# Performance work log

Measured on AMD Instinct MI355X. Metric: run time of the kernel, lower is better.

The kernel has to match this reference:

```python
import jax, jax.numpy as jnp
import numpy as np

N_PATCH, N_Z, K, BS = 16, 128, 10, 1024
D = N_PATCH * N_Z


def setup_inputs() -> dict:
    key = jax.random.key(0)
    k1, k2, k3, k4 = jax.random.split(key, 4)
    z = jax.random.normal(k1, (BS, D), dtype=jnp.float32)
    m = jax.random.normal(k2, (K, D), dtype=jnp.float32)
    L = jax.random.normal(k3, (K, D, D), dtype=jnp.float32)
    components = jax.random.randint(k4, (BS,), 0, K, dtype=jnp.int64)
    return {"z": z, "m": m, "L": L, "components": components}


def reference(z, m, L, components):
    # samps[k] = m[k] + z @ L[k].T   -> (K, BS, D)
    samps = jnp.einsum('bd,ked->kbe', z, L) + m[:, None, :]
    # one-hot mask-and-sum over components == gather selected expert per sample
    x = samps[components, jnp.arange(z.shape[0])]  # (BS, D)
    return x.reshape(-1, N_PATCH, N_Z)
```

## Files before the change

### kernel.cpp

```cpp
#include <hip/hip_runtime.h>
#include <hip/hip_bf16.h>


#define DDIM  2048
#define BSAMP 1024
#define KCOMP 10
#define MPAD  160
#define NT    32
#define BK    32
#define NITER (DDIM / BK)
#define TILEP 12288
#define ABYTES 12288
#define BBYTES 4096
#define STAGE_BYTES (ABYTES + BBYTES)
#define NBUF  3

typedef __attribute__((ext_vector_type(8))) short bf16x8;
typedef __attribute__((ext_vector_type(4))) float f32x4;

__device__ __forceinline__ void async16(void* lds, const void* g) {
    __builtin_amdgcn_global_load_lds(
        (const __attribute__((address_space(1))) void*)g,
        (__attribute__((address_space(3))) void*)lds, 16, 0, 0);
}

__device__ __forceinline__ short bfs(float x) {
    __hip_bfloat16 h = __float2bfloat16(x);
    return *reinterpret_cast<short*>(&h);
}

__global__ void build_map(const int* __restrict__ comp,
                          int* __restrict__ rowmap,
                          int* __restrict__ counts) {
    __shared__ int sc[KCOMP];
    const int t = threadIdx.x;
    if (t < KCOMP) sc[t] = 0;
    __syncthreads();
    const int c = comp[t];
    const int r = atomicAdd(&sc[c], 1);
    if (r < MPAD) rowmap[c * MPAD + r] = t;
    __syncthreads();
    if (t < KCOMP) counts[t] = sc[t];
}

__global__ void zgather(const float* __restrict__ z,
                        const int* __restrict__ rowmap,
                        short* __restrict__ zb) {
    const int k  = blockIdx.x;
    const int sp = blockIdx.y;
    const int t  = threadIdx.x;
    const int c  = t & 7;
    const int g  = c & 3;
    const int s0 = rowmap[k * MPAD + 2 * sp]     & (BSAMP - 1);
    const int s1 = rowmap[k * MPAD + 2 * sp + 1] & (BSAMP - 1);
    const int src = (c >> 2) ? s1 : s0;
    const int swz = (c ^ (sp & 7)) * 16;
    char* kbase = (char*)zb + (size_t)k * NITER * TILEP + sp * 128 + swz;
#pragma unroll
    for (int p = 0; p < 2; ++p) {
        const int it = p * 32 + (t >> 3);
        const float* zr = z + (size_t)src * DDIM + it * BK + g * 8;
        f32x4 x = *(const f32x4*)zr;
        f32x4 y = *(const f32x4*)(zr + 4);
        bf16x8 r;
#pragma unroll
        for (int i = 0; i < 4; ++i) { r[i] = bfs(x[i]); r[4 + i] = bfs(y[i]); }
        *(bf16x8*)(kbase + (size_t)it * TILEP) = r;
    }
}

__global__ __launch_bounds__(256, 3)
void gmm_gemm(const short* __restrict__ zb,
              const float* __restrict__ mvec,
              const float* __restrict__ Lmat,
              const int* __restrict__ rowmap,
              const int* __restrict__ counts,
              float* __restrict__ out) {
    __shared__ __attribute__((aligned(16))) char smem[NBUF * STAGE_BYTES];
    const int t    = threadIdx.x;
    const int lane = t & 63;
    const int w    = t >> 6;
    const int mh   = w >> 1;
    const int nh   = w & 1;
    const int k    = blockIdx.y;
    const int n0   = blockIdx.x * NT;
    const float* Lk = Lmat + (size_t)k * DDIM * DDIM;
    const char* zt  = (const char*)zb + (size_t)k * NITER * TILEP;
    const int cnt  = counts[k];

    int mtmax = (cnt - mh * 80 + 15) >> 4;
    mtmax = mtmax < 0 ? 0 : (mtmax > 5 ? 5 : mtmax);

    const int br = t >> 3,          bc = ((t & 7) ^ (br & 7)) * 4;
    const unsigned ub = (unsigned)(t & ~63) * 16;

    auto stage = [&](int bi, int it) {
        char* lb = smem + bi * STAGE_BYTES;
        const char* at = zt + (size_t)it * TILEP;
        async16(lb + ub,          at + t * 16);
        async16(lb + 4096 + ub,   at + 4096 + t * 16);
        async16(lb + 8192 + ub,   at + 8192 + t * 16);
        async16(lb + ABYTES + ub, Lk + (size_t)(n0 + br) * DDIM + it * BK + bc);
    };

    f32x4 acc[5];
#pragma unroll
    for (int mt = 0; mt < 5; ++mt) acc[mt] = (f32x4){0.f, 0.f, 0.f, 0.f};

    const int fr = lane & 15;
    const int g  = lane >> 4;
    const int rb = nh * 16 + fr;
    const int h0 = ((2 * g)     ^ (rb & 7)) * 4;
    const int h1 = ((2 * g + 1) ^ (rb & 7)) * 4;
    const int frh = fr >> 1;
    const int fra = (fr & 1) * 4 + g;
    const int abase = (mh * 40 + frh) * 128 + ((fra ^ frh) * 16);

    auto compute = [&](int bi) {
        const char* lb = smem + bi * STAGE_BYTES;
        const float* B = (const float*)(lb + ABYTES);
        f32x4 x = *(const f32x4*)(B + rb * 32 + h0);
        f32x4 y = *(const f32x4*)(B + rb * 32 + h1);
        bf16x8 bb;
#pragma unroll
        for (int i = 0; i < 4; ++i) { bb[i] = bfs(x[i]); bb[4 + i] = bfs(y[i]); }
#pragma unroll
        for (int mt = 0; mt < 5; ++mt) {
            if (mt < mtmax) {
                bf16x8 a = *(const bf16x8*)(lb + abase + mt * 1024);
                acc[mt] = __builtin_amdgcn_mfma_f32_16x16x32_bf16(a, bb, acc[mt], 0, 0, 0);
            }
        }
    };

    stage(0, 0); stage(1, 1); stage(2, 2);
    int bi = 0;
    for (int it = 0; it < NITER - 2; ++it) {
        asm volatile("s_waitcnt vmcnt(8)" ::: "memory");
        __builtin_amdgcn_s_barrier();
        compute(bi);
        __builtin_amdgcn_s_barrier();
        if (it + 3 < NITER) stage(bi, it + 3);
        bi = (bi == NBUF - 1) ? 0 : bi + 1;
    }
    asm volatile("s_waitcnt vmcnt(4)" ::: "memory");
    __builtin_amdgcn_s_barrier();
    compute(bi);
    __builtin_amdgcn_s_barrier();
    bi = (bi == NBUF - 1) ? 0 : bi + 1;
    asm volatile("s_waitcnt vmcnt(0)" ::: "memory");
    __builtin_amdgcn_s_barrier();
    compute(bi);

    const int rquad = g * 4;
    const int e  = n0 + nh * 16 + fr;
    const float mu = mvec[k * DDIM + e];
#pragma unroll
    for (int mt = 0; mt < 5; ++mt) {
        if (mt < mtmax) {
            const int sb = mh * 80 + mt * 16 + rquad;
#pragma unroll
            for (int r = 0; r < 4; ++r) {
                const int slot = sb + r;
                if (slot < cnt) {
                    const int b = rowmap[k * MPAD + slot];
                    out[(size_t)b * DDIM + e] = acc[mt][r] + mu;
                }
            }
        }
    }
}

extern "C" void kernel_launch(void* const* d_in, const int* in_sizes, int n_in,
                              void* d_out, int out_size, void* d_ws, size_t ws_size,
                              hipStream_t stream) {
    const float* z    = (const float*)d_in[0];
    const float* mvec = (const float*)d_in[1];
    const float* Lmat = (const float*)d_in[2];
    const int* comp   = (const int*)d_in[3];
    float* out        = (float*)d_out;

    int* rowmap = (int*)d_ws;
    int* counts = rowmap + KCOMP * MPAD;
    short* zb   = (short*)((char*)d_ws + 8192);

    build_map<<<1, BSAMP, 0, stream>>>(comp, rowmap, counts);
    zgather<<<dim3(KCOMP, MPAD / 2), 256, 0, stream>>>(z, rowmap, zb);
    gmm_gemm<<<dim3(DDIM / NT, KCOMP), 256, 0, stream>>>(zb, mvec, Lmat,
                                                         rowmap, counts, out);
}
```

Measured before the change: 271.3 us.

## Widen GEMM N tile to 128 with 512-thread blocks and 2x N fragments

Each block now covers 128 output columns instead of 32, using 8 waves. Each wave accumulates two 16-wide N fragments, so every A-fragment read from LDS feeds two MFMAs. The z-tile staged in LDS is now amortised over four times as many L columns, which cuts redundant A loads. In exchange the grid shrinks from 640 to 160 blocks on a 256-CU part, so the card may be underfilled, and each block uses 96KB of LDS at one block per CU. The kernel is dominated by streaming L, so that underfill may hurt bandwidth.

```diff
diff --git a/kernel.cpp b/kernel.cpp
--- a/kernel.cpp
+++ b/kernel.cpp
@@ -6,13 +6,12 @@
 #define BSAMP 1024
 #define KCOMP 10
 #define MPAD  160
-#define NT    32
+#define NT    128
 #define BK    32
 #define NITER (DDIM / BK)
 #define TILEP 12288
-#define ABYTES 12288
-#define BBYTES 4096
-#define STAGE_BYTES (ABYTES + BBYTES)
+#define ALDS  16384
+#define STAGE_BYTES 32768
 #define NBUF  3
 
 typedef __attribute__((ext_vector_type(8))) short bf16x8;
@@ -69,7 +68,7 @@
     }
 }
 
-__global__ __launch_bounds__(256, 3)
+__global__ __launch_bounds__(512, 1)
 void gmm_gemm(const short* __restrict__ zb,
               const float* __restrict__ mvec,
               const float* __restrict__ Lmat,
@@ -80,8 +79,8 @@
     const int t    = threadIdx.x;
     const int lane = t & 63;
     const int w    = t >> 6;
-    const int mh   = w >> 1;
-    const int nh   = w & 1;
+    const int mh   = w & 1;
+    const int nq   = w >> 1;
     const int k    = blockIdx.y;
     const int n0   = blockIdx.x * NT;
     const float* Lk = Lmat + (size_t)k * DDIM * DDIM;
@@ -91,44 +90,59 @@
     int mtmax = (cnt - mh * 80 + 15) >> 4;
     mtmax = mtmax < 0 ? 0 : (mtmax > 5 ? 5 : mtmax);
 
-    const int br = t >> 3,          bc = ((t & 7) ^ (br & 7)) * 4;
+    const int br0 = t >> 3,        bc0 = ((t & 7) ^ (br0 & 7)) * 4;
+    const int c1  = 512 + t;
+    const int br1 = c1 >> 3,       bc1 = ((c1 & 7) ^ (br1 & 7)) * 4;
+    const int ac1 = (512 + t < 640) ? (512 + t) : 639;
     const unsigned ub = (unsigned)(t & ~63) * 16;
 
     auto stage = [&](int bi, int it) {
         char* lb = smem + bi * STAGE_BYTES;
         const char* at = zt + (size_t)it * TILEP;
-        async16(lb + ub,          at + t * 16);
-        async16(lb + 4096 + ub,   at + 4096 + t * 16);
-        async16(lb + 8192 + ub,   at + 8192 + t * 16);
-        async16(lb + ABYTES + ub, Lk + (size_t)(n0 + br) * DDIM + it * BK + bc);
+        async16(lb + ub,               at + t * 16);
+        async16(lb + 8192 + ub,        at + ac1 * 16);
+        async16(lb + ALDS + ub,        Lk + (size_t)(n0 + br0) * DDIM + it * BK + bc0);
+        async16(lb + ALDS + 8192 + ub, Lk + (size_t)(n0 + br1) * DDIM + it * BK + bc1);
     };
 
-    f32x4 acc[5];
-#pragma unroll
-    for (int mt = 0; mt < 5; ++mt) acc[mt] = (f32x4){0.f, 0.f, 0.f, 0.f};
+    f32x4 acc[5][2];
+#pragma unroll
+    for (int mt = 0; mt < 5; ++mt) {
+        acc[mt][0] = (f32x4){0.f, 0.f, 0.f, 0.f};
+        acc[mt][1] = (f32x4){0.f, 0.f, 0.f, 0.f};
+    }
 
     const int fr = lane & 15;
     const int g  = lane >> 4;
-    const int rb = nh * 16 + fr;
-    const int h0 = ((2 * g)     ^ (rb & 7)) * 4;
-    const int h1 = ((2 * g + 1) ^ (rb & 7)) * 4;
+    const int rb0 = nq * 32 + fr;
+    const int rb1 = rb0 + 16;
+    const int h00 = ((2 * g)     ^ (rb0 & 7)) * 4;
+    const int h01 = ((2 * g + 1) ^ (rb0 & 7)) * 4;
+    const int h10 = ((2 * g)     ^ (rb1 & 7)) * 4;
+    const int h11 = ((2 * g + 1) ^ (rb1 & 7)) * 4;
     const int frh = fr >> 1;
     const int fra = (fr & 1) * 4 + g;
     const int abase = (mh * 40 + frh) * 128 + ((fra ^ frh) * 16);
 
     auto compute = [&](int bi) {
         const char* lb = smem + bi * STAGE_BYTES;
-        const float* B = (const float*)(lb + ABYTES);
-        f32x4 x = *(const f32x4*)(B + rb * 32 + h0);
-        f32x4 y = *(const f32x4*)(B + rb * 32 + h1);
-        bf16x8 bb;
-#pragma unroll
-        for (int i = 0; i < 4; ++i) { bb[i] = bfs(x[i]); bb[4 + i] = bfs(y[i]); }
+        const float* B = (const float*)(lb + ALDS);
+        f32x4 x0 = *(const f32x4*)(B + rb0 * 32 + h00);
+        f32x4 y0 = *(const f32x4*)(B + rb0 * 32 + h01);
+        f32x4 x1 = *(const f32x4*)(B + rb1 * 32 + h10);
+        f32x4 y1 = *(const f32x4*)(B + rb1 * 32 + h11);
+        bf16x8 b0, b1;
+#pragma unroll
+        for (int i = 0; i < 4; ++i) {
+            b0[i] = bfs(x0[i]); b0[4 + i] = bfs(y0[i]);
+            b1[i] = bfs(x1[i]); b1[4 + i] = bfs(y1[i]);
+        }
 #pragma unroll
         for (int mt = 0; mt < 5; ++mt) {
             if (mt < mtmax) {
                 bf16x8 a = *(const bf16x8*)(lb + abase + mt * 1024);
-                acc[mt] = __builtin_amdgcn_mfma_f32_16x16x32_bf16(a, bb, acc[mt], 0, 0, 0);
+                acc[mt][0] = __builtin_amdgcn_mfma_f32_16x16x32_bf16(a, b0, acc[mt][0], 0, 0, 0);
+                acc[mt][1] = __builtin_amdgcn_mfma_f32_16x16x32_bf16(a, b1, acc[mt][1], 0, 0, 0);
             }
         }
     };
@@ -153,18 +167,21 @@
     compute(bi);
 
     const int rquad = g * 4;
-    const int e  = n0 + nh * 16 + fr;
-    const float mu = mvec[k * DDIM + e];
-#pragma unroll
-    for (int mt = 0; mt < 5; ++mt) {
-        if (mt < mtmax) {
-            const int sb = mh * 80 + mt * 16 + rquad;
-#pragma unroll
-            for (int r = 0; r < 4; ++r) {
-                const int slot = sb + r;
-                if (slot < cnt) {
-                    const int b = rowmap[k * MPAD + slot];
-                    out[(size_t)b * DDIM + e] = acc[mt][r] + mu;
+#pragma unroll
+    for (int nt16 = 0; nt16 < 2; ++nt16) {
+        const int e = n0 + nq * 32 + nt16 * 16 + fr;
+        const float mu = mvec[k * DDIM + e];
+#pragma unroll
+        for (int mt = 0; mt < 5; ++mt) {
+            if (mt < mtmax) {
+                const int sb = mh * 80 + mt * 16 + rquad;
+#pragma unroll
+                for (int r = 0; r < 4; ++r) {
+                    const int slot = sb + r;
+                    if (slot < cnt) {
+                        const int b = rowmap[k * MPAD + slot];
+                        out[(size_t)b * DDIM + e] = acc[mt][nt16][r] + mu;
+                    }
                 }
             }
         }
@@ -186,6 +203,6 @@
 
     build_map<<<1, BSAMP, 0, stream>>>(comp, rowmap, counts);
     zgather<<<dim3(KCOMP, MPAD / 2), 256, 0, stream>>>(z, rowmap, zb);
-    gmm_gemm<<<dim3(DDIM / NT, KCOMP), 256, 0, stream>>>(zb, mvec, Lmat,
+    gmm_gemm<<<dim3(DDIM / NT, KCOMP), 512, 0, stream>>>(zb, mvec, Lmat,
                                                          rowmap, counts, out);
 }
```

Result: no change. 268.4 us (-1.1%).
